# Kernel optimization log

Hardware: AMD Instinct MI355X
Metric: run time of the kernel (lower is better)

The kernel has to match this reference:

```python
import jax, jax.numpy as jnp
import numpy as np

B, N, L, C, H = 2, 3000, 6, 128, 1
IN_DIM = 6
SIGMA_D = 1.0
EPS = 1e-5
DH = C // H


def _conv1(x, W, b):
    # pointwise Conv1d: x [B,Cin,N], W [Cout,Cin], b [Cout]
    return jnp.einsum('oc,bcn->bon', W, x) + b[None, :, None]


def _bn(x, g, beta):
    # BatchNorm1d (training-mode batch stats) over (B, N) per channel
    m = x.mean(axis=(0, 2), keepdims=True)
    v = x.var(axis=(0, 2), keepdims=True)
    return g[None, :, None] * (x - m) * jax.lax.rsqrt(v + EPS) + beta[None, :, None]


def setup_inputs() -> dict:
    key = jax.random.key(0)
    ks = iter(jax.random.split(key, 80))

    def w(shape, fan_in):
        return jax.random.normal(next(ks), shape, jnp.float32) * (1.0 / np.sqrt(fan_in))

    src = jax.random.normal(next(ks), (B, N, 3), jnp.float32)
    tgt = src + 0.1 * jax.random.normal(next(ks), (B, N, 3), jnp.float32)
    corr_pos = jnp.concatenate([src, tgt], axis=-1)  # [B,N,6]

    d = {
        'corr_pos': corr_pos, 'src_keypts': src, 'tgt_keypts': tgt,
        'init_W': w((C, IN_DIM), IN_DIM), 'init_b': jnp.zeros((C,), jnp.float32),
        'pcn_W': w((L, C, C), C), 'pcn_b': jnp.zeros((L, C), jnp.float32),
        'pcn_g': jnp.ones((L, C), jnp.float32), 'pcn_beta': jnp.zeros((L, C), jnp.float32),
        'qW': w((L, C, C), C), 'qb': jnp.zeros((L, C), jnp.float32),
        'kW': w((L, C, C), C), 'kb': jnp.zeros((L, C), jnp.float32),
        'vW': w((L, C, C), C), 'vb': jnp.zeros((L, C), jnp.float32),
        'm1W': w((L, C // 2, C), C), 'm1b': jnp.zeros((L, C // 2), jnp.float32),
        'm1g': jnp.ones((L, C // 2), jnp.float32), 'm1beta': jnp.zeros((L, C // 2), jnp.float32),
        'm2W': w((L, C // 2, C // 2), C // 2), 'm2b': jnp.zeros((L, C // 2), jnp.float32),
        'm2g': jnp.ones((L, C // 2), jnp.float32), 'm2beta': jnp.zeros((L, C // 2), jnp.float32),
        'm3W': w((L, C, C // 2), C // 2), 'm3b': jnp.zeros((L, C), jnp.float32),
        'c1W': w((32, C), C), 'c1b': jnp.zeros((32,), jnp.float32),
        'c2W': w((32, 32), 32), 'c2b': jnp.zeros((32,), jnp.float32),
        'c3W': w((1, 32), 32), 'c3b': jnp.zeros((1,), jnp.float32),
    }
    return d


def reference(corr_pos, src_keypts, tgt_keypts, init_W, init_b,
              pcn_W, pcn_b, pcn_g, pcn_beta,
              qW, qb, kW, kb, vW, vb,
              m1W, m1b, m1g, m1beta, m2W, m2b, m2g, m2beta, m3W, m3b,
              c1W, c1b, c2W, c2b, c3W, c3b):
    # spatial compatibility: clamp(1 - (d_src - d_tgt)^2 / sigma_d^2, min=0)  [B,N,N]
    src_dist = jnp.linalg.norm(src_keypts[:, :, None, :] - src_keypts[:, None, :, :], axis=-1)
    tgt_dist = jnp.linalg.norm(tgt_keypts[:, :, None, :] - tgt_keypts[:, None, :, :], axis=-1)
    sc = jnp.maximum(1.0 - (src_dist - tgt_dist) ** 2 / SIGMA_D ** 2, 0.0)

    # init embedding: [B,C,N]
    x = _conv1(jnp.swapaxes(corr_pos, 1, 2), init_W, init_b)
    scale = 1.0 / jnp.sqrt(jnp.float32(DH))

    for i in range(L):
        # PointCN layer
        x = jax.nn.relu(_bn(_conv1(x, pcn_W[i], pcn_b[i]), pcn_g[i], pcn_beta[i]))
        # NonLocal block
        Q = _conv1(x, qW[i], qb[i]).reshape(B, H, DH, N)
        K = _conv1(x, kW[i], kb[i]).reshape(B, H, DH, N)
        V = _conv1(x, vW[i], vb[i]).reshape(B, H, DH, N)
        scores = jnp.einsum('bhco,bhci->bhoi', Q, K) * scale  # [B,H,N,N]
        weight = jax.nn.softmax(sc[:, None, :, :] * scores, axis=-1)
        msg = jnp.einsum('bhoi,bhci->bhco', weight, V).reshape(B, C, N)
        msg = jax.nn.relu(_bn(_conv1(msg, m1W[i], m1b[i]), m1g[i], m1beta[i]))
        msg = jax.nn.relu(_bn(_conv1(msg, m2W[i], m2b[i]), m2g[i], m2beta[i]))
        msg = _conv1(msg, m3W[i], m3b[i])
        x = x + msg

    corr_feat = x
    norm = jnp.maximum(jnp.linalg.norm(corr_feat, axis=1, keepdims=True), 1e-12)
    normed_corr_feat = corr_feat / norm
    h = jax.nn.relu(_conv1(corr_feat, c1W, c1b))
    h = jax.nn.relu(_conv1(h, c2W, c2b))
    confidence = _conv1(h, c3W, c3b)[:, 0, :]  # [B,N]
    return confidence, normed_corr_feat
```

## Files before the change

### kernel.cpp

```cpp
#include <hip/hip_runtime.h>
#include <hip/hip_bf16.h>


#define BB 2
#define NN 3000
#define CC 128
#define LAYERS 6
#define BN_EPS 1e-5f
#define ATT_SCALE 0.08838834764831845f

typedef _Float16 f16;
typedef _Float16 f16x8 __attribute__((ext_vector_type(8)));
typedef float f32x4 __attribute__((ext_vector_type(4)));

__global__ void init_conv(const float* __restrict__ corr, const float* __restrict__ W,
                          const float* __restrict__ bias, float* __restrict__ x) {
  int idx = blockIdx.x * 256 + threadIdx.x;
  if (idx >= BB * CC * NN) return;
  int n = idx % NN;
  int c = (idx / NN) % CC;
  int b = idx / (NN * CC);
  const float* cp = corr + (b * NN + n) * 6;
  float acc = bias[c];
#pragma unroll
  for (int d = 0; d < 6; ++d) acc += W[c * 6 + d] * cp[d];
  x[idx] = acc;
}

template <int CIN, int COUT, int MODE, int INPT, int CSPLIT, int BNIN>
__launch_bounds__(256)
__global__ void conv_k(const float* __restrict__ in, float* __restrict__ out,
                       const float* __restrict__ W, const float* __restrict__ bias,
                       const float* __restrict__ res, const float* __restrict__ bns,
                       const float* __restrict__ bnr) {
  constexpr int COB = COUT / CSPLIT;
  constexpr int CH = (CIN > 64) ? 64 : CIN;
  constexpr int KPT = COB / 32;
  __shared__ alignas(16) float Xs[CIN][INPT ? 36 : 32];
  __shared__ float Ws[COB][CH + 1];
  const int tid = threadIdx.x;
  const int p0 = blockIdx.x * 32;
  const int co0 = blockIdx.y * COB;

  if (INPT == 0) {
    for (int idx = tid; idx < CIN * 32; idx += 256) {
      int ci = idx >> 5, j = idx & 31;
      int p = p0 + j;
      float v = 0.f;
      if (p < BB * NN) {
        int b = p / NN, n = p % NN;
        v = in[(b * CIN + ci) * NN + n];
        if (BNIN) {
          v = v * bns[ci] + bns[CIN + ci];
          v = v > 0.f ? v : 0.f;
        }
      }
      Xs[ci][j] = v;
    }
  } else {
    for (int idx = tid; idx < CIN * 32; idx += 256) {
      int j = idx / CIN, ci = idx % CIN;
      int p = p0 + j;
      float v = 0.f;
      if (p < BB * NN) {
        v = in[p * CIN + ci];
        if (BNIN) {
          v = v * bns[ci] + bns[CIN + ci];
          v = v > 0.f ? v : 0.f;
        }
      }
      Xs[ci][j] = v;
    }
  }

  const int nb = (tid % 8) * 4;
  const int cb = (tid / 8) * KPT;

  float acc[KPT][4];
#pragma unroll
  for (int k = 0; k < KPT; ++k)
#pragma unroll
    for (int j = 0; j < 4; ++j) acc[k][j] = 0.f;

  for (int c0 = 0; c0 < CIN; c0 += CH) {
    __syncthreads();
    for (int idx = tid; idx < COB * CH; idx += 256) {
      int co = idx / CH, cc = idx % CH;
      Ws[co][cc] = W[(co0 + co) * CIN + c0 + cc];
    }
    __syncthreads();
#pragma unroll 4
    for (int cc = 0; cc < CH; ++cc) {
      float4 xv = *reinterpret_cast<const float4*>(&Xs[c0 + cc][nb]);
#pragma unroll
      for (int k = 0; k < KPT; ++k) {
        float w = Ws[cb + k][cc];
        acc[k][0] += w * xv.x;
        acc[k][1] += w * xv.y;
        acc[k][2] += w * xv.z;
        acc[k][3] += w * xv.w;
      }
    }
  }

#pragma unroll
  for (int k = 0; k < KPT; ++k) {
    int co = co0 + cb + k;
    float bv = bias[co];
    float rsc = 0.f, rsh = 0.f;
    if (MODE == 3) {
      rsc = bnr[co];
      rsh = bnr[COUT + co];
    }
#pragma unroll
    for (int j = 0; j < 4; ++j) {
      int p = p0 + nb + j;
      if (p < BB * NN) {
        int b = p / NN, n = p % NN;
        int o = (b * COUT + co) * NN + n;
        float v = acc[k][j] + bv;
        if (MODE == 1) v = v > 0.f ? v : 0.f;
        if (MODE == 2) v += res[o];
        if (MODE == 3) {
          float rr = res[o] * rsc + rsh;
          v += (rr > 0.f ? rr : 0.f);
        }
        out[o] = v;
      }
    }
  }
}

__launch_bounds__(256)
__global__ void conv_qkv(const float* __restrict__ Yp, const float* __restrict__ bns,
                         const float* __restrict__ qW, const float* __restrict__ kW,
                         const float* __restrict__ vW, const float* __restrict__ qb,
                         const float* __restrict__ kb, const float* __restrict__ vb,
                         f16* __restrict__ Qh, f16* __restrict__ Ql,
                         f16* __restrict__ Kh, f16* __restrict__ Kl,
                         f16* __restrict__ Vh, f16* __restrict__ Vl) {
  __shared__ alignas(16) float Xs[128][32];
  __shared__ float Ws[64][65];
  const int tid = threadIdx.x;
  const int p0 = blockIdx.x * 32;
  const int sel = blockIdx.y >> 1;
  const int co0 = (blockIdx.y & 1) * 64;
  const float* W = (sel == 0) ? qW : (sel == 1) ? kW : vW;
  const float* bias = (sel == 0) ? qb : (sel == 1) ? kb : vb;

  for (int idx = tid; idx < 128 * 32; idx += 256) {
    int ci = idx >> 5, j = idx & 31;
    int p = p0 + j;
    float v = 0.f;
    if (p < BB * NN) {
      int b = p / NN, n = p % NN;
      v = Yp[(b * 128 + ci) * NN + n];
      v = v * bns[ci] + bns[128 + ci];
      v = v > 0.f ? v : 0.f;
    }
    Xs[ci][j] = v;
  }

  const int nb = (tid % 8) * 4;
  const int cb = (tid / 8) * 2;
  float acc[2][4] = {{0.f, 0.f, 0.f, 0.f}, {0.f, 0.f, 0.f, 0.f}};

  for (int c0 = 0; c0 < 128; c0 += 64) {
    __syncthreads();
    for (int idx = tid; idx < 64 * 64; idx += 256) {
      int co = idx >> 6, cc = idx & 63;
      Ws[co][cc] = W[(co0 + co) * 128 + c0 + cc];
    }
    __syncthreads();
#pragma unroll 4
    for (int cc = 0; cc < 64; ++cc) {
      float4 xv = *reinterpret_cast<const float4*>(&Xs[c0 + cc][nb]);
#pragma unroll
      for (int k = 0; k < 2; ++k) {
        float w = Ws[cb + k][cc];
        acc[k][0] += w * xv.x;
        acc[k][1] += w * xv.y;
        acc[k][2] += w * xv.z;
        acc[k][3] += w * xv.w;
      }
    }
  }

#pragma unroll
  for (int k = 0; k < 2; ++k) {
    int co = co0 + cb + k;
    float bv = bias[co];
#pragma unroll
    for (int j = 0; j < 4; ++j) {
      int p = p0 + nb + j;
      if (p < BB * NN) {
        int b = p / NN, n = p % NN;
        float v = acc[k][j] + bv;
        f16 h = (f16)v;
        f16 lo = (f16)(v - (float)h);
        if (sel == 0) {
          size_t o = (size_t)(b * NN + n) * CC + co;
          Qh[o] = h; Ql[o] = lo;
        } else if (sel == 1) {
          size_t o = (size_t)(b * NN + n) * CC + co;
          Kh[o] = h; Kl[o] = lo;
        } else {
          size_t o = (size_t)(b * CC + co) * NN + n;
          Vh[o] = h; Vl[o] = lo;
        }
      }
    }
  }
}

template <int COUT>
__launch_bounds__(256)
__global__ void bn_stats(const float* __restrict__ y, const float* __restrict__ g,
                         const float* __restrict__ beta, float* __restrict__ ss) {
  int c = blockIdx.x;
  float s = 0.f, s2 = 0.f;
  for (int b = 0; b < BB; ++b) {
    const float* row = y + (b * COUT + c) * NN;
    for (int n = threadIdx.x; n < NN; n += 256) {
      float v = row[n];
      s += v;
      s2 += v * v;
    }
  }
  for (int off = 32; off > 0; off >>= 1) {
    s += __shfl_down(s, off);
    s2 += __shfl_down(s2, off);
  }
  __shared__ float rs[4], rs2[4];
  int wid = threadIdx.x >> 6, lane = threadIdx.x & 63;
  if (lane == 0) {
    rs[wid] = s;
    rs2[wid] = s2;
  }
  __syncthreads();
  if (threadIdx.x == 0) {
    float S = 0.f, S2 = 0.f;
    for (int w = 0; w < 4; ++w) {
      S += rs[w];
      S2 += rs2[w];
    }
    const float inv_cnt = 1.f / (float)(BB * NN);
    float mean = S * inv_cnt;
    float var = S2 * inv_cnt - mean * mean;
    float scale = g[c] * rsqrtf(var + BN_EPS);
    ss[c] = scale;
    ss[COUT + c] = beta[c] - mean * scale;
  }
}

__launch_bounds__(256)
__global__ void attn_mf6(const f16* __restrict__ Qhp, const f16* __restrict__ Qlp,
                         const f16* __restrict__ Khp, const f16* __restrict__ Klp,
                         const f16* __restrict__ Vhp, const f16* __restrict__ Vlp,
                         const float* __restrict__ srcp, const float* __restrict__ tgtp,
                         float* __restrict__ pacc, float* __restrict__ pm,
                         float* __restrict__ pl, int chunk) {
  const int b = blockIdx.z;
  const int q0 = blockIdx.x * 64;
  const int s = blockIdx.y;
  const int cs = s * chunk;
  const int ce = min(cs + chunk, NN);
  const int tid = threadIdx.x;
  const int w = tid >> 6, lane = tid & 63, quad = lane >> 4, l15 = lane & 15;

  __shared__ f16 Ksh[32][136], Ksl[32][136];
  __shared__ f16 Vsh[128][40], Vsl[128][40];
  __shared__ f16 Ps[4][16][40];
  __shared__ float kps[6][36];

  float qp[4][6];
  const int orow = q0 + w * 16;
#pragma unroll
  for (int r = 0; r < 4; ++r) {
    int o = orow + quad * 4 + r;
    if (o >= NN) o = NN - 1;
#pragma unroll
    for (int d = 0; d < 3; ++d) {
      qp[r][d] = srcp[(b * NN + o) * 3 + d];
      qp[r][3 + d] = tgtp[(b * NN + o) * 3 + d];
    }
  }
  f16x8 qh[4], ql[4];
  {
    int o = orow + l15;
    if (o >= NN) o = NN - 1;
    size_t base = (size_t)(b * NN + o) * CC + quad * 8;
#pragma unroll
    for (int cc = 0; cc < 4; ++cc) {
      qh[cc] = *reinterpret_cast<const f16x8*>(Qhp + base + cc * 32);
      ql[cc] = *reinterpret_cast<const f16x8*>(Qlp + base + cc * 32);
    }
  }

  float m[4], l[4];
#pragma unroll
  for (int r = 0; r < 4; ++r) {
    m[r] = -1e30f;
    l[r] = 0.f;
  }
  f32x4 acco[8];
#pragma unroll
  for (int t = 0; t < 8; ++t) acco[t] = (f32x4){0.f, 0.f, 0.f, 0.f};

  const int NT = (ce - cs + 31) >> 5;
  for (int it = 0; it < NT; ++it) {
    const int kk0 = cs + it * 32;
    __syncthreads();
    for (int t = tid; t < 1024; t += 256) {
      int plane = t >> 9, row = (t >> 4) & 31, cu = t & 15;
      int kr = kk0 + row;
      if (kr >= NN) kr = NN - 1;
      const f16* src = (plane ? Klp : Khp) + (size_t)(b * NN + kr) * CC + cu * 8;
      uint4 v = *reinterpret_cast<const uint4*>(src);
      f16* dst = plane ? &Ksl[row][cu * 8] : &Ksh[row][cu * 8];
      *reinterpret_cast<uint4*>(dst) = v;
    }
    for (int t = tid; t < 1024; t += 256) {
      int plane = t >> 9, c = (t >> 2) & 127, iu = t & 3;
      int kb = kk0 + iu * 8;
      if (kb > NN - 8) kb = NN - 8;
      const f16* src = (plane ? Vlp : Vhp) + (size_t)(b * CC + c) * NN + kb;
      uint4 v = *reinterpret_cast<const uint4*>(src);
      f16* dst = plane ? &Vsl[c][iu * 8] : &Vsh[c][iu * 8];
      *reinterpret_cast<uint4*>(dst) = v;
    }
    for (int t = tid; t < 192; t += 256) {
      int d = t >> 5, i = t & 31;
      int ig = kk0 + i;
      if (ig >= NN) ig = NN - 1;
      kps[d][i] = (d < 3) ? srcp[(b * NN + ig) * 3 + d] : tgtp[(b * NN + ig) * 3 + d - 3];
    }
    __syncthreads();

    f32x4 accs[2];
#pragma unroll
    for (int k4 = 0; k4 < 2; ++k4) accs[k4] = (f32x4){0.f, 0.f, 0.f, 0.f};
#pragma unroll
    for (int cc = 0; cc < 4; ++cc) {
#pragma unroll
      for (int k4 = 0; k4 < 2; ++k4) {
        f16x8 bh = *reinterpret_cast<const f16x8*>(&Ksh[k4 * 16 + l15][cc * 32 + quad * 8]);
        f16x8 bl = *reinterpret_cast<const f16x8*>(&Ksl[k4 * 16 + l15][cc * 32 + quad * 8]);
        accs[k4] = __builtin_amdgcn_mfma_f32_16x16x32_f16(qh[cc], bl, accs[k4], 0, 0, 0);
        accs[k4] = __builtin_amdgcn_mfma_f32_16x16x32_f16(ql[cc], bh, accs[k4], 0, 0, 0);
        accs[k4] = __builtin_amdgcn_mfma_f32_16x16x32_f16(qh[cc], bh, accs[k4], 0, 0, 0);
      }
    }

    float sv[2][4];
#pragma unroll
    for (int k4 = 0; k4 < 2; ++k4) {
      int iloc = k4 * 16 + l15;
      int ig = kk0 + iloc;
      float kx = kps[0][iloc], ky = kps[1][iloc], kz = kps[2][iloc];
      float tx = kps[3][iloc], ty = kps[4][iloc], tz = kps[5][iloc];
#pragma unroll
      for (int r = 0; r < 4; ++r) {
        float dx = qp[r][0] - kx, dy = qp[r][1] - ky, dz = qp[r][2] - kz;
        float ds2 = dx * dx + dy * dy + dz * dz;
        float ex = qp[r][3] - tx, ey = qp[r][4] - ty, ez = qp[r][5] - tz;
        float dt2 = ex * ex + ey * ey + ez * ez;
        float d2 = ds2 + dt2 - 2.f * sqrtf(ds2 * dt2);
        float gg = 1.f - d2;
        gg = gg > 0.f ? gg : 0.f;
        float val = accs[k4][r] * (ATT_SCALE * gg);
        sv[k4][r] = (ig < ce) ? val : -1e30f;
      }
    }

    float tmax[4];
#pragma unroll
    for (int r = 0; r < 4; ++r) tmax[r] = fmaxf(sv[0][r], sv[1][r]);
#pragma unroll
    for (int d = 1; d <= 8; d <<= 1)
#pragma unroll
      for (int r = 0; r < 4; ++r) tmax[r] = fmaxf(tmax[r], __shfl_xor(tmax[r], d));

    float alpha[4], ps[4];
    f16 pf[2][4];
#pragma unroll
    for (int r = 0; r < 4; ++r) {
      float mn = fmaxf(m[r], tmax[r]);
      alpha[r] = __expf(m[r] - mn);
      m[r] = mn;
      pf[0][r] = (f16)__expf(sv[0][r] - mn);
      pf[1][r] = (f16)__expf(sv[1][r] - mn);
      ps[r] = (float)pf[0][r] + (float)pf[1][r];
    }
#pragma unroll
    for (int d = 1; d <= 8; d <<= 1)
#pragma unroll
      for (int r = 0; r < 4; ++r) ps[r] += __shfl_xor(ps[r], d);
#pragma unroll
    for (int r = 0; r < 4; ++r) {
      l[r] = l[r] * alpha[r] + ps[r];
#pragma unroll
      for (int t = 0; t < 8; ++t) acco[t][r] *= alpha[r];
    }
#pragma unroll
    for (int r = 0; r < 4; ++r) {
      Ps[w][quad * 4 + r][l15] = pf[0][r];
      Ps[w][quad * 4 + r][16 + l15] = pf[1][r];
    }
    __syncthreads();

    {
      f16x8 af = *reinterpret_cast<const f16x8*>(&Ps[w][l15][quad * 8]);
#pragma unroll
      for (int t = 0; t < 8; ++t) {
        f16x8 vh = *reinterpret_cast<const f16x8*>(&Vsh[t * 16 + l15][quad * 8]);
        f16x8 vl = *reinterpret_cast<const f16x8*>(&Vsl[t * 16 + l15][quad * 8]);
        acco[t] = __builtin_amdgcn_mfma_f32_16x16x32_f16(af, vl, acco[t], 0, 0, 0);
        acco[t] = __builtin_amdgcn_mfma_f32_16x16x32_f16(af, vh, acco[t], 0, 0, 0);
      }
    }
  }

  const int pidx = s * BB + b;
  if (l15 == 0) {
#pragma unroll
    for (int r = 0; r < 4; ++r) {
      int o = orow + quad * 4 + r;
      if (o < NN) {
        pm[pidx * NN + o] = m[r];
        pl[pidx * NN + o] = l[r];
      }
    }
  }
#pragma unroll
  for (int r = 0; r < 4; ++r) {
    int o = orow + quad * 4 + r;
    if (o < NN) {
      size_t base2 = ((size_t)pidx * NN + o) * CC;
#pragma unroll
      for (int t = 0; t < 8; ++t) pacc[base2 + t * 16 + l15] = acco[t][r];
    }
  }
}

__launch_bounds__(256)
__global__ void conv_m1(const float* __restrict__ pacc, const float* __restrict__ pm,
                        const float* __restrict__ pl, float* __restrict__ out,
                        const float* __restrict__ W, const float* __restrict__ bias,
                        int ksplit) {
  __shared__ alignas(16) float Xs[128][36];
  __shared__ float Ws[64][65];
  __shared__ float Es[32][9];
  __shared__ float Li[32];
  const int tid = threadIdx.x;
  const int p0 = blockIdx.x * 32;

  if (tid < 32) {
    int p = p0 + tid;
    float Lv = 1.f;
    if (p < BB * NN) {
      int b = p / NN, o = p % NN;
      float M = -1e30f;
      for (int s = 0; s < ksplit; ++s) M = fmaxf(M, pm[(s * BB + b) * NN + o]);
      Lv = 0.f;
      for (int s = 0; s < ksplit; ++s) {
        int pi = s * BB + b;
        float e = __expf(pm[pi * NN + o] - M);
        Es[tid][s] = e;
        Lv += pl[pi * NN + o] * e;
      }
    } else {
      for (int s = 0; s < ksplit; ++s) Es[tid][s] = 0.f;
    }
    Li[tid] = 1.f / Lv;
  }
  __syncthreads();

  for (int idx = tid; idx < 1024; idx += 256) {
    int j = idx >> 5, c4 = (idx & 31) * 4;
    int p = p0 + j;
    float4 a = {0.f, 0.f, 0.f, 0.f};
    if (p < BB * NN) {
      int b = p / NN, o = p % NN;
      for (int s = 0; s < ksplit; ++s) {
        float e = Es[j][s];
        const float4 pv = *reinterpret_cast<const float4*>(
            &pacc[((size_t)(s * BB + b) * NN + o) * CC + c4]);
        a.x += pv.x * e;
        a.y += pv.y * e;
        a.z += pv.z * e;
        a.w += pv.w * e;
      }
      float inv = Li[j];
      a.x *= inv; a.y *= inv; a.z *= inv; a.w *= inv;
    }
    Xs[c4][j] = a.x;
    Xs[c4 + 1][j] = a.y;
    Xs[c4 + 2][j] = a.z;
    Xs[c4 + 3][j] = a.w;
  }

  const int nb = (tid % 8) * 4;
  const int cb = (tid / 8) * 2;
  float acc[2][4] = {{0.f, 0.f, 0.f, 0.f}, {0.f, 0.f, 0.f, 0.f}};

  for (int c0 = 0; c0 < 128; c0 += 64) {
    __syncthreads();
    for (int idx = tid; idx < 64 * 64; idx += 256) {
      int co = idx >> 6, cc = idx & 63;
      Ws[co][cc] = W[co * 128 + c0 + cc];
    }
    __syncthreads();
#pragma unroll 4
    for (int cc = 0; cc < 64; ++cc) {
      float4 xv = *reinterpret_cast<const float4*>(&Xs[c0 + cc][nb]);
#pragma unroll
      for (int k = 0; k < 2; ++k) {
        float w = Ws[cb + k][cc];
        acc[k][0] += w * xv.x;
        acc[k][1] += w * xv.y;
        acc[k][2] += w * xv.z;
        acc[k][3] += w * xv.w;
      }
    }
  }

#pragma unroll
  for (int k = 0; k < 2; ++k) {
    int co = cb + k;
    float bv = bias[co];
#pragma unroll
    for (int j = 0; j < 4; ++j) {
      int p = p0 + nb + j;
      if (p < BB * NN) {
        int b = p / NN, n = p % NN;
        out[(b * 64 + co) * NN + n] = acc[k][j] + bv;
      }
    }
  }
}

__launch_bounds__(256)
__global__ void head_all(const float* __restrict__ Xg,
                         const float* __restrict__ c1W, const float* __restrict__ c1b,
                         const float* __restrict__ c2W, const float* __restrict__ c2b,
                         const float* __restrict__ c3W, const float* __restrict__ c3b,
                         float* __restrict__ out) {
  __shared__ float Xs[128][33];
  __shared__ float W1[32][129];
  __shared__ float W2[32][33];
  __shared__ float Hs[32][33], H2s[32][33];
  __shared__ float Inv[32];
  const int tid = threadIdx.x;
  const int p0 = blockIdx.x * 32;
  const int j = tid >> 3, sub = tid & 7;

  for (int idx = tid; idx < 128 * 32; idx += 256) {
    int ci = idx >> 5, jj = idx & 31;
    int p = p0 + jj;
    float v = 0.f;
    if (p < BB * NN) {
      int b = p / NN, n = p % NN;
      v = Xg[(b * 128 + ci) * NN + n];
    }
    Xs[ci][jj] = v;
  }
  for (int idx = tid; idx < 32 * 128; idx += 256) {
    W1[idx >> 7][idx & 127] = c1W[idx];
  }
  for (int idx = tid; idx < 32 * 32; idx += 256) {
    W2[idx >> 5][idx & 31] = c2W[idx];
  }
  __syncthreads();

  {
    float h1v[4];
#pragma unroll
    for (int k = 0; k < 4; ++k) h1v[k] = c1b[sub * 4 + k];
    for (int ci = 0; ci < 128; ++ci) {
      float xv = Xs[ci][j];
#pragma unroll
      for (int k = 0; k < 4; ++k) h1v[k] += W1[sub * 4 + k][ci] * xv;
    }
#pragma unroll
    for (int k = 0; k < 4; ++k) Hs[j][sub * 4 + k] = h1v[k] > 0.f ? h1v[k] : 0.f;
  }
  __syncthreads();
  {
    float h2v[4];
#pragma unroll
    for (int k = 0; k < 4; ++k) h2v[k] = c2b[sub * 4 + k];
#pragma unroll
    for (int cc = 0; cc < 32; ++cc) {
      float hv = Hs[j][cc];
#pragma unroll
      for (int k = 0; k < 4; ++k) h2v[k] += W2[sub * 4 + k][cc] * hv;
    }
#pragma unroll
    for (int k = 0; k < 4; ++k) H2s[j][sub * 4 + k] = h2v[k] > 0.f ? h2v[k] : 0.f;
  }
  __syncthreads();

  float ssp = 0.f;
#pragma unroll
  for (int k = 0; k < 16; ++k) {
    float v = Xs[sub + 8 * k][j];
    ssp += v * v;
  }
  ssp += __shfl_xor(ssp, 1);
  ssp += __shfl_xor(ssp, 2);
  ssp += __shfl_xor(ssp, 4);

  if (sub == 0) {
    int p = p0 + j;
    if (p < BB * NN) {
      float conf = c3b[0];
#pragma unroll
      for (int c = 0; c < 32; ++c) conf += c3W[c] * H2s[j][c];
      out[p] = conf;
    }
    float nrm = sqrtf(ssp);
    nrm = nrm > 1e-12f ? nrm : 1e-12f;
    Inv[j] = 1.f / nrm;
  }
  __syncthreads();

  for (int idx = tid; idx < 128 * 32; idx += 256) {
    int c = idx >> 5, jj = idx & 31;
    int p = p0 + jj;
    if (p < BB * NN) {
      int b = p / NN, n = p % NN;
      out[BB * NN + (b * 128 + c) * NN + n] = Xs[c][jj] * Inv[jj];
    }
  }
}

extern "C" void kernel_launch(void* const* d_in, const int* in_sizes, int n_in,
                              void* d_out, int out_size, void* d_ws, size_t ws_size,
                              hipStream_t stream) {
  const float* corr = (const float*)d_in[0];
  const float* srcp = (const float*)d_in[1];
  const float* tgtp = (const float*)d_in[2];
  const float* initW = (const float*)d_in[3];
  const float* initb = (const float*)d_in[4];
  const float* pcnW = (const float*)d_in[5];
  const float* pcnb = (const float*)d_in[6];
  const float* pcng = (const float*)d_in[7];
  const float* pcnbeta = (const float*)d_in[8];
  const float* qW = (const float*)d_in[9];
  const float* qb = (const float*)d_in[10];
  const float* kW = (const float*)d_in[11];
  const float* kb = (const float*)d_in[12];
  const float* vW = (const float*)d_in[13];
  const float* vb = (const float*)d_in[14];
  const float* m1W = (const float*)d_in[15];
  const float* m1b = (const float*)d_in[16];
  const float* m1g = (const float*)d_in[17];
  const float* m1beta = (const float*)d_in[18];
  const float* m2W = (const float*)d_in[19];
  const float* m2b = (const float*)d_in[20];
  const float* m2g = (const float*)d_in[21];
  const float* m2beta = (const float*)d_in[22];
  const float* m3W = (const float*)d_in[23];
  const float* m3b = (const float*)d_in[24];
  const float* c1W = (const float*)d_in[25];
  const float* c1b = (const float*)d_in[26];
  const float* c2W = (const float*)d_in[27];
  const float* c2b = (const float*)d_in[28];
  const float* c3W = (const float*)d_in[29];
  const float* c3b = (const float*)d_in[30];

  const int FEAT = BB * CC * NN;
  const int PLANE = FEAT / 2;
  float* ws = (float*)d_ws;
  float* X = ws;
  float* Y = X + FEAT;
  float* QhF = Y + FEAT;
  float* QlF = QhF + PLANE;
  float* KhF = QlF + PLANE;
  float* KlF = KhF + PLANE;
  float* VhF = KlF + PLANE;
  float* VlF = VhF + PLANE;
  float* SSp = VlF + PLANE;
  float* SSa = SSp + 256;
  float* SSb = SSa + 256;
  float* pacc = SSb + 256;
  f16* Qh = (f16*)QhF;
  f16* Ql = (f16*)QlF;
  f16* Kh = (f16*)KhF;
  f16* Kl = (f16*)KlF;
  f16* Vh = (f16*)VhF;
  f16* Vl = (f16*)VlF;
  float* T1 = QhF;
  float* T2 = KhF;

  const size_t base_f = (size_t)(2 * FEAT + 6 * PLANE + 768);
  const size_t per_f = (size_t)BB * NN * CC + 2 * (size_t)BB * NN;
  int ksplit = 8;
  while (ksplit > 1 && (base_f + (size_t)ksplit * per_f) * 4 > ws_size) ksplit >>= 1;
  const int chunk = (((NN + ksplit - 1) / ksplit) + 7) & ~7;
  float* pm = pacc + (size_t)ksplit * BB * NN * CC;
  float* pl = pm + (size_t)ksplit * BB * NN;

  dim3 blk(256);
  const int PT = (BB * NN + 31) / 32;
  const int G_FEAT = (FEAT + 255) / 256;

  init_conv<<<G_FEAT, blk, 0, stream>>>(corr, initW, initb, X);

  for (int i = 0; i < LAYERS; ++i) {
    conv_k<128, 128, 0, 0, 2, 0><<<dim3(PT, 2), blk, 0, stream>>>(
        X, Y, pcnW + i * 16384, pcnb + i * 128, nullptr, nullptr, nullptr);
    bn_stats<128><<<128, blk, 0, stream>>>(Y, pcng + i * 128, pcnbeta + i * 128, SSp);
    conv_qkv<<<dim3(PT, 6), blk, 0, stream>>>(Y, SSp, qW + i * 16384, kW + i * 16384,
                                              vW + i * 16384, qb + i * 128, kb + i * 128,
                                              vb + i * 128, Qh, Ql, Kh, Kl, Vh, Vl);
    attn_mf6<<<dim3((NN + 63) / 64, ksplit, BB), blk, 0, stream>>>(
        Qh, Ql, Kh, Kl, Vh, Vl, srcp, tgtp, pacc, pm, pl, chunk);
    conv_m1<<<PT, blk, 0, stream>>>(pacc, pm, pl, T1, m1W + i * 8192, m1b + i * 64,
                                    ksplit);
    bn_stats<64><<<64, blk, 0, stream>>>(T1, m1g + i * 64, m1beta + i * 64, SSa);
    conv_k<64, 64, 0, 0, 1, 1><<<dim3(PT, 1), blk, 0, stream>>>(
        T1, T2, m2W + i * 4096, m2b + i * 64, nullptr, SSa, nullptr);
    bn_stats<64><<<64, blk, 0, stream>>>(T2, m2g + i * 64, m2beta + i * 64, SSb);
    conv_k<64, 128, 3, 0, 2, 1><<<dim3(PT, 2), blk, 0, stream>>>(
        T2, X, m3W + i * 8192, m3b + i * 128, Y, SSb, SSp);
  }

  head_all<<<PT, blk, 0, stream>>>(X, c1W, c1b, c2W, c2b, c3W, c3b, (float*)d_out);
}
```

Baseline: 1.521 ms.

## Fuse BatchNorm statistics into conv epilogues via atomics, drop bn_stats kernels

Each conv that feeds a BatchNorm now reduces per-channel sum and sum-of-squares in its epilogue, using wave shuffles and then atomicAdd into a zeroed per-layer buffer. Consumer kernels turn those sums into scale and shift themselves. This removes the three separate bn_stats launches per layer and their extra reads of the activations. The m2 conv is also split across two channel blocks for more parallelism. The cost is atomic contention, one memset per call, and nondeterministic float summation order.

After: 1.508 ms. Within noise of the previous version (-0.8%).

```diff
diff --git a/kernel.cpp b/kernel.cpp
--- a/kernel.cpp
+++ b/kernel.cpp
@@ -8,6 +8,7 @@
 #define LAYERS 6
 #define BN_EPS 1e-5f
 #define ATT_SCALE 0.08838834764831845f
+#define INV_CNT (1.f / (float)(BB * NN))
 
 typedef _Float16 f16;
 typedef _Float16 f16x8 __attribute__((ext_vector_type(8)));
@@ -27,20 +28,36 @@
   x[idx] = acc;
 }
 
-template <int CIN, int COUT, int MODE, int INPT, int CSPLIT, int BNIN>
+template <int CIN, int COUT, int MODE, int INPT, int CSPLIT, int BNIN, int STATS>
 __launch_bounds__(256)
 __global__ void conv_k(const float* __restrict__ in, float* __restrict__ out,
                        const float* __restrict__ W, const float* __restrict__ bias,
-                       const float* __restrict__ res, const float* __restrict__ bns,
-                       const float* __restrict__ bnr) {
+                       const float* __restrict__ res,
+                       const float* __restrict__ isums, const float* __restrict__ ig,
+                       const float* __restrict__ ibeta,
+                       const float* __restrict__ rsums, const float* __restrict__ rg,
+                       const float* __restrict__ rbeta, float* __restrict__ osums) {
   constexpr int COB = COUT / CSPLIT;
   constexpr int CH = (CIN > 64) ? 64 : CIN;
   constexpr int KPT = COB / 32;
   __shared__ alignas(16) float Xs[CIN][INPT ? 36 : 32];
   __shared__ float Ws[COB][CH + 1];
+  __shared__ float bnsc[BNIN ? CIN : 1], bnsh[BNIN ? CIN : 1];
   const int tid = threadIdx.x;
   const int p0 = blockIdx.x * 32;
   const int co0 = blockIdx.y * COB;
+
+  if (BNIN) {
+    for (int c = tid; c < CIN; c += 256) {
+      float s = isums[c], s2 = isums[CIN + c];
+      float mean = s * INV_CNT;
+      float var = s2 * INV_CNT - mean * mean;
+      float sc = ig[c] * rsqrtf(var + BN_EPS);
+      bnsc[c] = sc;
+      bnsh[c] = ibeta[c] - mean * sc;
+    }
+    __syncthreads();
+  }
 
   if (INPT == 0) {
     for (int idx = tid; idx < CIN * 32; idx += 256) {
@@ -51,7 +68,7 @@
         int b = p / NN, n = p % NN;
         v = in[(b * CIN + ci) * NN + n];
         if (BNIN) {
-          v = v * bns[ci] + bns[CIN + ci];
+          v = v * bnsc[ci] + bnsh[ci];
           v = v > 0.f ? v : 0.f;
         }
       }
@@ -65,7 +82,7 @@
       if (p < BB * NN) {
         v = in[p * CIN + ci];
         if (BNIN) {
-          v = v * bns[ci] + bns[CIN + ci];
+          v = v * bnsc[ci] + bnsh[ci];
           v = v > 0.f ? v : 0.f;
         }
       }
@@ -109,9 +126,13 @@
     float bv = bias[co];
     float rsc = 0.f, rsh = 0.f;
     if (MODE == 3) {
-      rsc = bnr[co];
-      rsh = bnr[COUT + co];
-    }
+      float s = rsums[co], s2 = rsums[COUT + co];
+      float mean = s * INV_CNT;
+      float var = s2 * INV_CNT - mean * mean;
+      rsc = rg[co] * rsqrtf(var + BN_EPS);
+      rsh = rbeta[co] - mean * rsc;
+    }
+    float sp = 0.f, sp2 = 0.f;
 #pragma unroll
     for (int j = 0; j < 4; ++j) {
       int p = p0 + nb + j;
@@ -120,19 +141,35 @@
         int o = (b * COUT + co) * NN + n;
         float v = acc[k][j] + bv;
         if (MODE == 1) v = v > 0.f ? v : 0.f;
-        if (MODE == 2) v += res[o];
         if (MODE == 3) {
           float rr = res[o] * rsc + rsh;
           v += (rr > 0.f ? rr : 0.f);
         }
         out[o] = v;
+        if (STATS) {
+          sp += v;
+          sp2 += v * v;
+        }
+      }
+    }
+    if (STATS) {
+      sp += __shfl_xor(sp, 1);
+      sp2 += __shfl_xor(sp2, 1);
+      sp += __shfl_xor(sp, 2);
+      sp2 += __shfl_xor(sp2, 2);
+      sp += __shfl_xor(sp, 4);
+      sp2 += __shfl_xor(sp2, 4);
+      if ((tid & 7) == 0) {
+        atomicAdd(&osums[co], sp);
+        atomicAdd(&osums[COUT + co], sp2);
       }
     }
   }
 }
 
 __launch_bounds__(256)
-__global__ void conv_qkv(const float* __restrict__ Yp, const float* __restrict__ bns,
+__global__ void conv_qkv(const float* __restrict__ Yp, const float* __restrict__ psums,
+                         const float* __restrict__ pg, const float* __restrict__ pbeta,
                          const float* __restrict__ qW, const float* __restrict__ kW,
                          const float* __restrict__ vW, const float* __restrict__ qb,
                          const float* __restrict__ kb, const float* __restrict__ vb,
@@ -141,12 +178,23 @@
                          f16* __restrict__ Vh, f16* __restrict__ Vl) {
   __shared__ alignas(16) float Xs[128][32];
   __shared__ float Ws[64][65];
+  __shared__ float bnsc[128], bnsh[128];
   const int tid = threadIdx.x;
   const int p0 = blockIdx.x * 32;
   const int sel = blockIdx.y >> 1;
   const int co0 = (blockIdx.y & 1) * 64;
   const float* W = (sel == 0) ? qW : (sel == 1) ? kW : vW;
   const float* bias = (sel == 0) ? qb : (sel == 1) ? kb : vb;
+
+  for (int c = tid; c < 128; c += 256) {
+    float s = psums[c], s2 = psums[128 + c];
+    float mean = s * INV_CNT;
+    float var = s2 * INV_CNT - mean * mean;
+    float sc = pg[c] * rsqrtf(var + BN_EPS);
+    bnsc[c] = sc;
+    bnsh[c] = pbeta[c] - mean * sc;
+  }
+  __syncthreads();
 
   for (int idx = tid; idx < 128 * 32; idx += 256) {
     int ci = idx >> 5, j = idx & 31;
@@ -155,7 +203,7 @@
     if (p < BB * NN) {
       int b = p / NN, n = p % NN;
       v = Yp[(b * 128 + ci) * NN + n];
-      v = v * bns[ci] + bns[128 + ci];
+      v = v * bnsc[ci] + bnsh[ci];
       v = v > 0.f ? v : 0.f;
     }
     Xs[ci][j] = v;
@@ -213,46 +261,6 @@
   }
 }
 
-template <int COUT>
-__launch_bounds__(256)
-__global__ void bn_stats(const float* __restrict__ y, const float* __restrict__ g,
-                         const float* __restrict__ beta, float* __restrict__ ss) {
-  int c = blockIdx.x;
-  float s = 0.f, s2 = 0.f;
-  for (int b = 0; b < BB; ++b) {
-    const float* row = y + (b * COUT + c) * NN;
-    for (int n = threadIdx.x; n < NN; n += 256) {
-      float v = row[n];
-      s += v;
-      s2 += v * v;
-    }
-  }
-  for (int off = 32; off > 0; off >>= 1) {
-    s += __shfl_down(s, off);
-    s2 += __shfl_down(s2, off);
-  }
-  __shared__ float rs[4], rs2[4];
-  int wid = threadIdx.x >> 6, lane = threadIdx.x & 63;
-  if (lane == 0) {
-    rs[wid] = s;
-    rs2[wid] = s2;
-  }
-  __syncthreads();
-  if (threadIdx.x == 0) {
-    float S = 0.f, S2 = 0.f;
-    for (int w = 0; w < 4; ++w) {
-      S += rs[w];
-      S2 += rs2[w];
-    }
-    const float inv_cnt = 1.f / (float)(BB * NN);
-    float mean = S * inv_cnt;
-    float var = S2 * inv_cnt - mean * mean;
-    float scale = g[c] * rsqrtf(var + BN_EPS);
-    ss[c] = scale;
-    ss[COUT + c] = beta[c] - mean * scale;
-  }
-}
-
 __launch_bounds__(256)
 __global__ void attn_mf6(const f16* __restrict__ Qhp, const f16* __restrict__ Qlp,
                          const f16* __restrict__ Khp, const f16* __restrict__ Klp,
@@ -447,7 +455,7 @@
 __global__ void conv_m1(const float* __restrict__ pacc, const float* __restrict__ pm,
                         const float* __restrict__ pl, float* __restrict__ out,
                         const float* __restrict__ W, const float* __restrict__ bias,
-                        int ksplit) {
+                        float* __restrict__ osums, int ksplit) {
   __shared__ alignas(16) float Xs[128][36];
   __shared__ float Ws[64][65];
   __shared__ float Es[32][9];
@@ -529,13 +537,27 @@
   for (int k = 0; k < 2; ++k) {
     int co = cb + k;
     float bv = bias[co];
+    float sp = 0.f, sp2 = 0.f;
 #pragma unroll
     for (int j = 0; j < 4; ++j) {
       int p = p0 + nb + j;
       if (p < BB * NN) {
         int b = p / NN, n = p % NN;
-        out[(b * 64 + co) * NN + n] = acc[k][j] + bv;
-      }
+        float v = acc[k][j] + bv;
+        out[(b * 64 + co) * NN + n] = v;
+        sp += v;
+        sp2 += v * v;
+      }
+    }
+    sp += __shfl_xor(sp, 1);
+    sp2 += __shfl_xor(sp2, 1);
+    sp += __shfl_xor(sp, 2);
+    sp2 += __shfl_xor(sp2, 2);
+    sp += __shfl_xor(sp, 4);
+    sp2 += __shfl_xor(sp2, 4);
+    if ((tid & 7) == 0) {
+      atomicAdd(&osums[co], sp);
+      atomicAdd(&osums[64 + co], sp2);
     }
   }
 }
@@ -681,10 +703,8 @@
   float* KlF = KhF + PLANE;
   float* VhF = KlF + PLANE;
   float* VlF = VhF + PLANE;
-  float* SSp = VlF + PLANE;
-  float* SSa = SSp + 256;
-  float* SSb = SSa + 256;
-  float* pacc = SSb + 256;
+  float* SB = VlF + PLANE;
+  float* pacc = SB + 3072;
   f16* Qh = (f16*)QhF;
   f16* Ql = (f16*)QlF;
   f16* Kh = (f16*)KhF;
@@ -694,7 +714,7 @@
   float* T1 = QhF;
   float* T2 = KhF;
 
-  const size_t base_f = (size_t)(2 * FEAT + 6 * PLANE + 768);
+  const size_t base_f = (size_t)(2 * FEAT + 6 * PLANE + 3072);
   const size_t per_f = (size_t)BB * NN * CC + 2 * (size_t)BB * NN;
   int ksplit = 8;
   while (ksplit > 1 && (base_f + (size_t)ksplit * per_f) * 4 > ws_size) ksplit >>= 1;
@@ -706,25 +726,31 @@
   const int PT = (BB * NN + 31) / 32;
   const int G_FEAT = (FEAT + 255) / 256;
 
+  hipMemsetAsync(SB, 0, 3072 * sizeof(float), stream);
   init_conv<<<G_FEAT, blk, 0, stream>>>(corr, initW, initb, X);
 
   for (int i = 0; i < LAYERS; ++i) {
-    conv_k<128, 128, 0, 0, 2, 0><<<dim3(PT, 2), blk, 0, stream>>>(
-        X, Y, pcnW + i * 16384, pcnb + i * 128, nullptr, nullptr, nullptr);
-    bn_stats<128><<<128, blk, 0, stream>>>(Y, pcng + i * 128, pcnbeta + i * 128, SSp);
-    conv_qkv<<<dim3(PT, 6), blk, 0, stream>>>(Y, SSp, qW + i * 16384, kW + i * 16384,
-                                              vW + i * 16384, qb + i * 128, kb + i * 128,
-                                              vb + i * 128, Qh, Ql, Kh, Kl, Vh, Vl);
+    float* pcnS = SB + i * 512;
+    float* m1S = pcnS + 256;
+    float* m2S = m1S + 128;
+    conv_k<128, 128, 0, 0, 2, 0, 1><<<dim3(PT, 2), blk, 0, stream>>>(
+        X, Y, pcnW + i * 16384, pcnb + i * 128, nullptr,
+        nullptr, nullptr, nullptr, nullptr, nullptr, nullptr, pcnS);
+    conv_qkv<<<dim3(PT, 6), blk, 0, stream>>>(
+        Y, pcnS, pcng + i * 128, pcnbeta + i * 128, qW + i * 16384, kW + i * 16384,
+        vW + i * 16384, qb + i * 128, kb + i * 128, vb + i * 128,
+        Qh, Ql, Kh, Kl, Vh, Vl);
     attn_mf6<<<dim3((NN + 63) / 64, ksplit, BB), blk, 0, stream>>>(
         Qh, Ql, Kh, Kl, Vh, Vl, srcp, tgtp, pacc, pm, pl, chunk);
     conv_m1<<<PT, blk, 0, stream>>>(pacc, pm, pl, T1, m1W + i * 8192, m1b + i * 64,
-                                    ksplit);
-    bn_stats<64><<<64, blk, 0, stream>>>(T1, m1g + i * 64, m1beta + i * 64, SSa);
-    conv_k<64, 64, 0, 0, 1, 1><<<dim3(PT, 1), blk, 0, stream>>>(
-        T1, T2, m2W + i * 4096, m2b + i * 64, nullptr, SSa, nullptr);
-    bn_stats<64><<<64, blk, 0, stream>>>(T2, m2g + i * 64, m2beta + i * 64, SSb);
-    conv_k<64, 128, 3, 0, 2, 1><<<dim3(PT, 2), blk, 0, stream>>>(
-        T2, X, m3W + i * 8192, m3b + i * 128, Y, SSb, SSp);
+                                    m1S, ksplit);
+    conv_k<64, 64, 0, 0, 2, 1, 1><<<dim3(PT, 2), blk, 0, stream>>>(
+        T1, T2, m2W + i * 4096, m2b + i * 64, nullptr,
+        m1S, m1g + i * 64, m1beta + i * 64, nullptr, nullptr, nullptr, m2S);
+    conv_k<64, 128, 3, 0, 2, 1, 0><<<dim3(PT, 2), blk, 0, stream>>>(
+        T2, X, m3W + i * 8192, m3b + i * 128, Y,
+        m2S, m2g + i * 64, m2beta + i * 64, pcnS, pcng + i * 128, pcnbeta + i * 128,
+        nullptr);
   }
 
   head_all<<<PT, blk, 0, stream>>>(X, c1W, c1b, c2W, c2b, c3W, c3b, (float*)d_out);
```
